# Kernel optimization log

Hardware: AMD Instinct MI355X
Metric: run time of the kernel (lower is better)

## Reference

```python
import jax, jax.numpy as jnp
import numpy as np

BN_EPS = 1e-5
EPS = 1e-6


def _conv(x, w, pad, dil):
    # NCHW dilated conv, stride 1, no bias (matches nn.Conv2d(bias=False))
    return jax.lax.conv_general_dilated(
        x, w, window_strides=(1, 1), padding=[(pad, pad), (pad, pad)],
        rhs_dilation=(dil, dil), dimension_numbers=('NCHW', 'OIHW', 'NCHW'))


def _bn_relu(x, s, b, m, v):
    # eval-mode batchnorm (running stats) + relu
    inv = (s / jnp.sqrt(v + BN_EPS))[None, :, None, None]
    return jax.nn.relu((x - m[None, :, None, None]) * inv + b[None, :, None, None])


def _l2n(x):
    # l2_norm over channel dim (dim=-2 of [B,C,N]); no eps, as in source
    return x / jnp.linalg.norm(x, axis=1, keepdims=True)


def _forward(x, w1, w2, w3, w4, bn_scale, bn_bias, bn_mean, bn_var,
             wq, bq, wk, bk, wv, bv, gamma):
    B, C, H, W = x.shape
    N = H * W
    # HASP: four dilated-conv branches (dilations 1,6,12,18), concat to 128 ch
    specs = [(w1, 0, 1), (w2, 6, 6), (w3, 12, 12), (w4, 18, 18)]
    branches = [_bn_relu(_conv(x, w, p, d), bn_scale[i], bn_bias[i],
                         bn_mean[i], bn_var[i])
                for i, (w, p, d) in enumerate(specs)]
    x_q = jnp.concatenate(branches, axis=1)  # [B,128,H,W]
    # 1x1 convs as channel GEMMs
    Q = (jnp.einsum('oi,bihw->bohw', wq[:, :, 0, 0], x_q)
         + bq[None, :, None, None]).reshape(B, -1, N)  # [B,16,N]
    K = (jnp.einsum('oi,bihw->bohw', wk[:, :, 0, 0], x)
         + bk[None, :, None, None]).reshape(B, -1, N)  # [B,16,N]
    V = (jnp.einsum('oi,bihw->bohw', wv[:, :, 0, 0], x)
         + bv[None, :, None, None]).reshape(B, -1, N)  # [B,128,N]
    Qn = _l2n(Q).transpose(0, 2, 1)  # [B,N,16]
    Kn = _l2n(K)                     # [B,16,N]
    tailor = 1.0 / (N + jnp.einsum('bnm,bm->bn', Qn, Kn.sum(-1) + EPS))  # [B,N]
    vsum = V.sum(-1)[:, :, None]                      # [B,128,1]
    mat = jnp.einsum('bmn,bcn->bmc', Kn, V)           # [B,16,128]
    msum = vsum + jnp.einsum('bnm,bmc->bcn', Qn, mat)  # [B,128,N]
    out = (msum * tailor[:, None, :]).reshape(B, C, H, W)
    return gamma * out


def setup_inputs() -> dict:
    key = jax.random.key(0)
    ks = jax.random.split(key, 12)
    B, C, H, W = 8, 128, 128, 128
    M = 16  # in_places // scale
    d = {
        'x': jax.random.normal(ks[0], (B, C, H, W), jnp.float32),
        'w1': jax.random.normal(ks[1], (32, 128, 1, 1), jnp.float32) * 0.05,
        'w2': jax.random.normal(ks[2], (32, 128, 3, 3), jnp.float32) * 0.05,
        'w3': jax.random.normal(ks[3], (32, 128, 3, 3), jnp.float32) * 0.05,
        'w4': jax.random.normal(ks[4], (32, 128, 3, 3), jnp.float32) * 0.05,
        'bn_scale': jnp.ones((4, 32), jnp.float32),
        'bn_bias': jnp.zeros((4, 32), jnp.float32),
        'bn_mean': jnp.zeros((4, 32), jnp.float32),
        'bn_var': jnp.ones((4, 32), jnp.float32),
        'wq': jax.random.normal(ks[5], (M, 128, 1, 1), jnp.float32) * 0.05,
        'bq': jax.random.normal(ks[6], (M,), jnp.float32) * 0.05,
        'wk': jax.random.normal(ks[7], (M, 128, 1, 1), jnp.float32) * 0.05,
        'bk': jax.random.normal(ks[8], (M,), jnp.float32) * 0.05,
        'wv': jax.random.normal(ks[9], (C, 128, 1, 1), jnp.float32) * 0.05,
        'bv': jax.random.normal(ks[10], (C,), jnp.float32) * 0.05,
        'gamma': jax.random.uniform(ks[11], (1,), jnp.float32),
    }
    return d


def reference(x, w1, w2, w3, w4, bn_scale, bn_bias, bn_mean, bn_var,
              wq, bq, wk, bk, wv, bv, gamma):
    return _forward(x, w1, w2, w3, w4, bn_scale, bn_bias, bn_mean, bn_var,
                    wq, bq, wk, bk, wv, bv, gamma)
```

## Files before the change

kernel.cpp:

```cpp
#include <hip/hip_runtime.h>
#include <hip/hip_bf16.h>
#include <math.h>

#define NPIX   16384
#define BATCH  8
#define BN_EPS 1e-5f
#define EPS_V  1e-6f

typedef __attribute__((ext_vector_type(8))) short bf16x8;
typedef __attribute__((ext_vector_type(4))) float f32x4;
typedef const __attribute__((address_space(1))) unsigned int* gas_ptr;
typedef __attribute__((address_space(3))) unsigned int* las_ptr;

#define OFF_K     ((size_t)0)
#define OFF_PART2 ((size_t)8192)
#define OFF_W1F   ((size_t)2097152)
#define OFF_WKT   ((size_t)2101248)
#define OFF_WVT   ((size_t)2103296)
#define OFF_BF    ((size_t)2119680)
#define OFF_PART  ((size_t)2119808)
#define OFF_STATS ((size_t)3242112)
#define BASE_END  ((size_t)3259648)
#define OFF_WBT   BASE_END
#define OFF_XT    ((size_t)3314976)
#define OFF_WVB   ((size_t)11703584)
#define OFF_ZROW  ((size_t)11711776)
#define NEW_END   ((size_t)11713824)
#define OFF_SQ    OFF_XT
#define OFF_TL    ((size_t)(OFF_XT + 2097152))
#define OFF_W24T  BASE_END

__device__ inline unsigned short f2bf(float f) {
  union { float f; unsigned int u; } v; v.f = f;
  unsigned int r = (v.u + 0x7FFFu + ((v.u >> 16) & 1u)) >> 16;
  return (unsigned short)r;
}

__global__ void prep_common_kernel(const float* __restrict__ w1,
                                   const float* __restrict__ bns, const float* __restrict__ bnb,
                                   const float* __restrict__ bnm, const float* __restrict__ bnv,
                                   const float* __restrict__ wk, const float* __restrict__ wv,
                                   float* __restrict__ w1f, float* __restrict__ wkt,
                                   float* __restrict__ wvt, float* __restrict__ bf) {
  int tid = blockIdx.x * blockDim.x + threadIdx.x;
  int nt  = gridDim.x * blockDim.x;
  for (int i = tid; i < 128; i += nt) {
    float inv = bns[i] * rsqrtf(bnv[i] + BN_EPS);
    bf[i] = bnb[i] - bnm[i] * inv;
  }
  for (int i = tid; i < 4096; i += nt) {
    int c = i >> 5, o = i & 31;
    float inv = bns[o] * rsqrtf(bnv[o] + BN_EPS);
    w1f[i] = w1[o * 128 + c] * inv;
  }
  for (int i = tid; i < 2048; i += nt) {
    int c = i >> 4, m = i & 15;
    wkt[i] = wk[m * 128 + c];
  }
  for (int i = tid; i < 16384; i += nt) {
    int c = i >> 7, o = i & 127;
    wvt[i] = wv[o * 128 + c];
  }
}

__global__ void prep_convb_kernel(const float* __restrict__ w1,
                                  const float* __restrict__ w2, const float* __restrict__ w3,
                                  const float* __restrict__ w4,
                                  const float* __restrict__ bns, const float* __restrict__ bnv,
                                  const float* __restrict__ wk, const float* __restrict__ wv,
                                  unsigned short* __restrict__ wbtr,
                                  unsigned short* __restrict__ wvbr,
                                  unsigned short* __restrict__ wxbr,
                                  unsigned short* __restrict__ zrow) {
  int tid = blockIdx.x * blockDim.x + threadIdx.x;
  int nt  = gridDim.x * blockDim.x;
  for (int i = tid; i < 4096; i += nt) zrow[i] = 0;
  for (int i = tid; i < 16384; i += nt) {
    int e = i & 7, lane = (i >> 3) & 63, f = (i >> 9) & 7, q = i >> 12;
    int oc = f * 16 + (lane & 15);
    int c  = q * 32 + (lane >> 4) * 8 + e;
    wvbr[i] = f2bf(wv[oc * 128 + c]);
  }
  for (int i = tid; i < 6144; i += nt) {
    int e = i & 7, lane = (i >> 3) & 63, ct = i >> 9;
    int tile = ct % 3, q = ct / 3;
    int c = q * 32 + (lane >> 4) * 8 + e;
    float val;
    if (tile < 2) {
      int oc = tile * 16 + (lane & 15);
      val = w1[oc * 128 + c] * (bns[oc] * rsqrtf(bnv[oc] + BN_EPS));
    } else {
      val = wk[(lane & 15) * 128 + c];
    }
    wxbr[i] = f2bf(val);
  }
  for (int i = tid; i < 110592; i += nt) {
    int br = i / 36864;
    int r  = i - br * 36864;
    int tap  = r >> 12;
    int r2   = r & 4095;
    int q    = r2 >> 10;
    int r3   = r2 & 1023;
    int pair = r3 >> 9;
    int r4   = r3 & 511;
    int lane = r4 >> 3, e = r4 & 7;
    int oc = pair * 16 + (lane & 15);
    int c  = q * 32 + (lane >> 4) * 8 + e;
    const float* w = (br == 0) ? w2 : ((br == 1) ? w3 : w4);
    int bo = (br + 1) * 32 + oc;
    float inv = bns[bo] * rsqrtf(bnv[bo] + BN_EPS);
    wbtr[i] = f2bf(w[(oc * 128 + c) * 9 + tap] * inv);
  }
}

__global__ void prep_convf_kernel(const float* __restrict__ w2, const float* __restrict__ w3,
                                  const float* __restrict__ w4,
                                  const float* __restrict__ bns, const float* __restrict__ bnv,
                                  float* __restrict__ w24t) {
  int tid = blockIdx.x * blockDim.x + threadIdx.x;
  int nt  = gridDim.x * blockDim.x;
  for (int i = tid; i < 110592; i += nt) {
    int br  = i / 36864;
    int rem = i - br * 36864;
    int c   = rem / 288;
    int k   = (rem % 288) >> 5;
    int o   = rem & 31;
    const float* w = (br == 0) ? w2 : ((br == 1) ? w3 : w4);
    int bo = (br + 1) * 32 + o;
    float inv = bns[bo] * rsqrtf(bnv[bo] + BN_EPS);
    w24t[i] = w[(o * 128 + c) * 9 + k] * inv;
  }
}

__global__ __launch_bounds__(256) void a0_kernel(const float* __restrict__ x,
                                                 unsigned short* __restrict__ xt) {
  __shared__ unsigned short Ts[64][132];
  int t   = threadIdx.x;
  int b   = blockIdx.y;
  int px0 = blockIdx.x * 64;
  const float* xb = x + (size_t)b * 128 * NPIX;
  int p = t & 63, cq = t >> 6;
#pragma unroll 8
  for (int i = 0; i < 32; ++i) {
    int c = cq * 32 + i;
    Ts[p][c] = f2bf(xb[(size_t)c * NPIX + px0 + p]);
  }
  __syncthreads();
  int pw = t >> 2, cg = t & 3;
  unsigned short* dst = xt + ((size_t)(b * 4 + cg) * 16384 + px0 + pw) * 32;
  int sw = (pw >> 1) & 3;
#pragma unroll
  for (int k = 0; k < 8; ++k) {
    uint2 v = *(const uint2*)(&Ts[pw][cg * 32 + k * 4]);
    int cgs = (k >> 1) ^ sw;
    *(uint2*)(dst + cgs * 8 + (k & 1) * 4) = v;
  }
}

__global__ __launch_bounds__(256) void a1_kernel(const float* __restrict__ x,
                                                 const float* __restrict__ w1f,
                                                 const float* __restrict__ wkt,
                                                 const float* __restrict__ bfp,
                                                 const float* __restrict__ bk,
                                                 float* __restrict__ out,
                                                 float* __restrict__ Kbuf) {
  __shared__ float lw1[128 * 32];
  __shared__ float lwk[128 * 16];
  __shared__ float lbf[32];
  int t = threadIdx.x;
  for (int i = t; i < 4096; i += 256) lw1[i] = w1f[i];
  for (int i = t; i < 2048; i += 256) lwk[i] = wkt[i];
  if (t < 32) lbf[t] = bfp[t];
  __syncthreads();

  int b  = blockIdx.y;
  int px = blockIdx.x * 256 + t;
  const float* xb = x + (size_t)b * 128 * NPIX;

  float acc[48];
#pragma unroll
  for (int i = 0; i < 48; ++i) acc[i] = 0.f;

  for (int c = 0; c < 128; ++c) {
    float xv = xb[(size_t)c * NPIX + px];
    const float4* w1p = (const float4*)(lw1 + c * 32);
#pragma unroll
    for (int j = 0; j < 8; ++j) {
      float4 w = w1p[j];
      acc[j*4+0] = fmaf(w.x, xv, acc[j*4+0]);
      acc[j*4+1] = fmaf(w.y, xv, acc[j*4+1]);
      acc[j*4+2] = fmaf(w.z, xv, acc[j*4+2]);
      acc[j*4+3] = fmaf(w.w, xv, acc[j*4+3]);
    }
    const float4* wkp = (const float4*)(lwk + c * 16);
#pragma unroll
    for (int j = 0; j < 4; ++j) {
      float4 w = wkp[j];
      acc[32+j*4+0] = fmaf(w.x, xv, acc[32+j*4+0]);
      acc[32+j*4+1] = fmaf(w.y, xv, acc[32+j*4+1]);
      acc[32+j*4+2] = fmaf(w.z, xv, acc[32+j*4+2]);
      acc[32+j*4+3] = fmaf(w.w, xv, acc[32+j*4+3]);
    }
  }
#pragma unroll
  for (int o = 0; o < 32; ++o)
    out[((size_t)(b * 128 + o)) * NPIX + px] = fmaxf(acc[o] + lbf[o], 0.f);
#pragma unroll
  for (int m = 0; m < 16; ++m)
    Kbuf[((size_t)(b * 16 + m)) * NPIX + px] = acc[32 + m] + bk[m];
}

__global__ __launch_bounds__(256) void a2m_kernel(const unsigned short* __restrict__ xt,
                                                  const unsigned short* __restrict__ zrow,
                                                  const unsigned short* __restrict__ wbtr,
                                                  const float* __restrict__ bfp,
                                                  float* __restrict__ out) {
  __shared__ unsigned short sx[3 * 8192 + 8];
  int t    = threadIdx.x;
  int wave = t >> 6, lane = t & 63;
  int l15  = lane & 15, cg = lane >> 4;
  int idx  = blockIdx.x;
  int b    = idx & 7;
  int rest = idx >> 3;
  int h2   = rest & 63;
  int br   = rest >> 6;
  int d    = 6 * (br + 1);
  int h0   = h2 * 2;
  int j    = wave >> 1;
  int whalf = wave & 1;
  int p0   = whalf * 64;

  if (t == 0) *(uint4*)(sx + 24576) = make_uint4(0u, 0u, 0u, 0u);

  const unsigned short* wb    = wbtr + (size_t)br * 36864;
  const unsigned short* slabs = xt + (size_t)b * 4 * 524288;

  f32x4 acc[2][4];
#pragma unroll
  for (int i = 0; i < 2; ++i)
#pragma unroll
    for (int n = 0; n < 4; ++n) acc[i][n] = (f32x4){0.f, 0.f, 0.f, 0.f};

  int pxb[3], xorv[3];
#pragma unroll
  for (int kw = 0; kw < 3; ++kw) {
    pxb[kw]  = p0 + l15 + (kw - 1) * d;
    xorv[kw] = (cg ^ ((pxb[kw] >> 1) & 3)) << 4;
  }

  auto STAGE = [&](int s) {
    int q = s / 3, kh = s % 3;
    int srow = h0 + j + (kh - 1) * d;
    const unsigned short* rowsrc =
        ((unsigned)srow < 128u) ? (slabs + (size_t)q * 524288 + (size_t)srow * 4096)
                                : zrow;
    const unsigned short* gsrc = rowsrc + whalf * 2048 + lane * 8;
    unsigned short* lbase = sx + (s % 3) * 8192 + j * 4096 + whalf * 2048;
#pragma unroll
    for (int k = 0; k < 4; ++k)
      __builtin_amdgcn_global_load_lds((gas_ptr)(const void*)(gsrc + k * 512),
                                       (las_ptr)(void*)(lbase + k * 512), 16, 0, 0);
  };

  auto COMPUTE = [&](int s) {
    int q = s / 3, kh = s % 3;
    int bb = (s % 3) * 16384 + j * 8192;
    bf16x8 a[3][2];
#pragma unroll
    for (int kw = 0; kw < 3; ++kw) {
      int tap = kh * 3 + kw;
      const unsigned short* wt = wb + ((((size_t)tap * 4 + q) * 2) << 9);
      a[kw][0] = *(const bf16x8*)(wt + lane * 8);
      a[kw][1] = *(const bf16x8*)(wt + 512 + lane * 8);
    }
#pragma unroll
    for (int kw = 0; kw < 3; ++kw) {
      int base = bb + pxb[kw] * 64 + xorv[kw];
#pragma unroll
      for (int nf = 0; nf < 4; ++nf) {
        int px   = pxb[kw] + nf * 16;
        int addr = ((unsigned)px < 128u) ? (base + nf * 1024) : 49152;
        bf16x8 bv = *(const bf16x8*)((const char*)sx + addr);
        acc[0][nf] = __builtin_amdgcn_mfma_f32_16x16x32_bf16(a[kw][0], bv, acc[0][nf], 0, 0, 0);
        acc[1][nf] = __builtin_amdgcn_mfma_f32_16x16x32_bf16(a[kw][1], bv, acc[1][nf], 0, 0, 0);
      }
    }
  };

  STAGE(0);
  __syncthreads();
  for (int s = 0; s < 12; ++s) {
    if (s < 11) STAGE(s + 1);
    COMPUTE(s);
    __syncthreads();
  }

  int ocb = (br + 1) * 32;
  int pxw = (h0 + j) * 128 + p0;
#pragma unroll
  for (int mf = 0; mf < 2; ++mf) {
#pragma unroll
    for (int r = 0; r < 4; ++r) {
      int oc = mf * 16 + cg * 4 + r;
      float bias = bfp[ocb + oc];
      float* op = out + ((size_t)(b * 128 + ocb + oc)) * NPIX + pxw + l15;
#pragma unroll
      for (int nf = 0; nf < 4; ++nf)
        op[nf * 16] = fmaxf(acc[mf][nf][r] + bias, 0.f);
    }
  }
}

__global__ __launch_bounds__(256) void a2f_kernel(const float* __restrict__ x,
                                                  const float* __restrict__ w24t,
                                                  const float* __restrict__ bfp,
                                                  float* __restrict__ out) {
  int t  = threadIdx.x;
  int og = t & 3;
  int pg = (t >> 2) & 15;
  int r  = t >> 6;
  int br = blockIdx.z;
  int b  = blockIdx.y;
  int h  = blockIdx.x * 4 + r;
  int d  = 6 * (br + 1);

  const float* wt = w24t + (size_t)br * 36864;
  const float* bf = bfp + (br + 1) * 32;
  const float* xb = x + (size_t)b * 128 * NPIX;
  int w0 = pg << 3;

  float acc[8][8];
#pragma unroll
  for (int p = 0; p < 8; ++p)
#pragma unroll
    for (int o = 0; o < 8; ++o) acc[p][o] = 0.f;

  for (int c = 0; c < 128; ++c) {
    const float* xc = xb + (size_t)c * NPIX;
    const float* wc = wt + c * 288;
#pragma unroll
    for (int kh = 0; kh < 3; ++kh) {
      int row = h + (kh - 1) * d;
      if ((unsigned)row >= 128u) continue;
      const float* xr = xc + row * 128;
#pragma unroll
      for (int kw = 0; kw < 3; ++kw) {
        int wb = w0 + (kw - 1) * d;
        float xv[8];
        if (wb >= 0 && wb <= 120) {
          const float2* p2 = (const float2*)(xr + wb);
#pragma unroll
          for (int jj = 0; jj < 4; ++jj) {
            float2 v = p2[jj];
            xv[2*jj] = v.x; xv[2*jj+1] = v.y;
          }
        } else {
#pragma unroll
          for (int jj = 0; jj < 8; ++jj) {
            int ww = wb + jj;
            xv[jj] = ((unsigned)ww < 128u) ? xr[ww] : 0.f;
          }
        }
        const float4* wp = (const float4*)(wc + (kh * 3 + kw) * 32 + og * 8);
        float4 wa = wp[0], wbv = wp[1];
        float wr[8] = {wa.x, wa.y, wa.z, wa.w, wbv.x, wbv.y, wbv.z, wbv.w};
#pragma unroll
        for (int p = 0; p < 8; ++p)
#pragma unroll
          for (int o = 0; o < 8; ++o)
            acc[p][o] = fmaf(xv[p], wr[o], acc[p][o]);
      }
    }
  }

  int chbase = (br + 1) * 32 + og * 8;
  int n = h * 128 + w0;
#pragma unroll
  for (int o = 0; o < 8; ++o) {
    float bias = bf[og * 8 + o];
    float* op = out + ((size_t)(b * 128 + chbase + o)) * NPIX + n;
    float4 v0 = make_float4(fmaxf(acc[0][o] + bias, 0.f), fmaxf(acc[1][o] + bias, 0.f),
                            fmaxf(acc[2][o] + bias, 0.f), fmaxf(acc[3][o] + bias, 0.f));
    float4 v1 = make_float4(fmaxf(acc[4][o] + bias, 0.f), fmaxf(acc[5][o] + bias, 0.f),
                            fmaxf(acc[6][o] + bias, 0.f), fmaxf(acc[7][o] + bias, 0.f));
    ((float4*)op)[0] = v0;
    ((float4*)op)[1] = v1;
  }
}

__global__ __launch_bounds__(256) void cm_kernel(const unsigned short* __restrict__ xt,
                                                 const unsigned short* __restrict__ wvbr,
                                                 const unsigned short* __restrict__ wxbr,
                                                 const float* __restrict__ bv,
                                                 const float* __restrict__ bfp,
                                                 const float* __restrict__ bk,
                                                 float* __restrict__ out,
                                                 float* __restrict__ part1,
                                                 float* __restrict__ part2) {
  __shared__ __align__(16) unsigned short Vl[128 * 136];
  __shared__ __align__(16) unsigned short knl[16 * 136];
  int t    = threadIdx.x;
  int idx  = blockIdx.x;
  int b    = idx & 7;
  int blk  = idx >> 3;
  int wave = t >> 6, lane = t & 63;
  int l15  = lane & 15, cg = lane >> 4;
  int ocb  = wave * 32;
  int pbase = blk << 7;
  int cgsw = (cg ^ ((l15 >> 1) & 3)) << 3;

  float bvr[2][4];
#pragma unroll
  for (int mf = 0; mf < 2; ++mf)
#pragma unroll
    for (int r = 0; r < 4; ++r) bvr[mf][r] = bv[ocb + mf * 16 + cg * 4 + r];

  float xb4[4];
#pragma unroll
  for (int r = 0; r < 4; ++r) xb4[r] = 0.f;
  if (wave == 0) {
#pragma unroll
    for (int r = 0; r < 4; ++r) xb4[r] = bfp[cg * 4 + r];
  } else if (wave == 1) {
#pragma unroll
    for (int r = 0; r < 4; ++r) xb4[r] = bfp[16 + cg * 4 + r];
  } else if (wave == 2) {
#pragma unroll
    for (int r = 0; r < 4; ++r) xb4[r] = bk[cg * 4 + r];
  }
  int xwave = (wave < 3) ? wave : 0;

  float kr[4] = {0.f, 0.f, 0.f, 0.f};
  float sv[2][4];
#pragma unroll
  for (int mf = 0; mf < 2; ++mf)
#pragma unroll
    for (int r = 0; r < 4; ++r) sv[mf][r] = 0.f;
  f32x4 am[2];
  am[0] = (f32x4){0.f,0.f,0.f,0.f};
  am[1] = (f32x4){0.f,0.f,0.f,0.f};

#pragma unroll
  for (int hf = 0; hf < 2; ++hf) {
    f32x4 vacc[2][4];
    f32x4 xacc[4];
#pragma unroll
    for (int i = 0; i < 2; ++i)
#pragma unroll
      for (int n = 0; n < 4; ++n) vacc[i][n] = (f32x4){0.f,0.f,0.f,0.f};
#pragma unroll
    for (int n = 0; n < 4; ++n) xacc[n] = (f32x4){0.f,0.f,0.f,0.f};

#pragma unroll
    for (int cc = 0; cc < 4; ++cc) {
      const unsigned short* xq = xt + ((size_t)(b * 4 + cc) * 16384 + pbase) * 32;
      bf16x8 a0 = *(const bf16x8*)(wvbr + ((cc * 8 + wave * 2 + 0) << 9) + lane * 8);
      bf16x8 a1 = *(const bf16x8*)(wvbr + ((cc * 8 + wave * 2 + 1) << 9) + lane * 8);
      bf16x8 ax = *(const bf16x8*)(wxbr + ((cc * 3 + xwave) << 9) + lane * 8);
#pragma unroll
      for (int nf = 0; nf < 4; ++nf) {
        int nfg = hf * 4 + nf;
        bf16x8 bx = *(const bf16x8*)(xq + (size_t)(nfg * 16 + l15) * 32 + cgsw);
        vacc[0][nf] = __builtin_amdgcn_mfma_f32_16x16x32_bf16(a0, bx, vacc[0][nf], 0, 0, 0);
        vacc[1][nf] = __builtin_amdgcn_mfma_f32_16x16x32_bf16(a1, bx, vacc[1][nf], 0, 0, 0);
        if (wave < 3)
          xacc[nf] = __builtin_amdgcn_mfma_f32_16x16x32_bf16(ax, bx, xacc[nf], 0, 0, 0);
      }
    }

#pragma unroll
    for (int mf = 0; mf < 2; ++mf) {
#pragma unroll
      for (int r = 0; r < 4; ++r) {
        float s = 0.f;
#pragma unroll
        for (int nf = 0; nf < 4; ++nf) s += vacc[mf][nf][r];
        sv[mf][r] += s;
        int c = ocb + mf * 16 + cg * 4 + r;
#pragma unroll
        for (int nf = 0; nf < 4; ++nf)
          Vl[c * 136 + (hf * 4 + nf) * 16 + l15] = f2bf(vacc[mf][nf][r] + bvr[mf][r]);
      }
    }

    if (wave < 2) {
#pragma unroll
      for (int r = 0; r < 4; ++r) {
        int oc = wave * 16 + cg * 4 + r;
        float* op = out + ((size_t)(b * 128 + oc)) * NPIX + pbase + l15;
#pragma unroll
        for (int nf = 0; nf < 4; ++nf)
          op[(hf * 4 + nf) * 16] = fmaxf(xacc[nf][r] + xb4[r], 0.f);
      }
    } else if (wave == 2) {
#pragma unroll
      for (int nf = 0; nf < 4; ++nf) {
        int nfg = hf * 4 + nf;
        float kq[4]; float s2 = 0.f;
#pragma unroll
        for (int r = 0; r < 4; ++r) {
          kq[r] = xacc[nf][r] + xb4[r];
          s2 = fmaf(kq[r], kq[r], s2);
        }
        s2 += __shfl_xor(s2, 16);
        s2 += __shfl_xor(s2, 32);
        float inv = rsqrtf(s2);
#pragma unroll
        for (int r = 0; r < 4; ++r) {
          float kn = kq[r] * inv;
          knl[(cg * 4 + r) * 136 + nfg * 16 + l15] = f2bf(kn);
          kr[r] += kn;
        }
      }
    }
  }
  __syncthreads();

#pragma unroll
  for (int ks = 0; ks < 4; ++ks) {
    bf16x8 af = *(const bf16x8*)(knl + l15 * 136 + ks * 32 + cg * 8);
    bf16x8 b0 = *(const bf16x8*)(Vl + (size_t)(ocb + l15) * 136 + ks * 32 + cg * 8);
    bf16x8 b1 = *(const bf16x8*)(Vl + (size_t)(ocb + 16 + l15) * 136 + ks * 32 + cg * 8);
    am[0] = __builtin_amdgcn_mfma_f32_16x16x32_bf16(af, b0, am[0], 0, 0, 0);
    am[1] = __builtin_amdgcn_mfma_f32_16x16x32_bf16(af, b1, am[1], 0, 0, 0);
  }

  float* pp = (blk < 64) ? (part1 + ((size_t)b * 64 + blk) * 2192)
                         : (part2 + ((size_t)b * 64 + (blk - 64)) * 2192);
#pragma unroll
  for (int nf2 = 0; nf2 < 2; ++nf2)
#pragma unroll
    for (int r = 0; r < 4; ++r)
      pp[(cg * 4 + r) * 128 + ocb + nf2 * 16 + l15] = am[nf2][r];
#pragma unroll
  for (int off = 1; off < 16; off <<= 1) {
#pragma unroll
    for (int mf = 0; mf < 2; ++mf)
#pragma unroll
      for (int r = 0; r < 4; ++r)
        sv[mf][r] += __shfl_xor(sv[mf][r], off);
  }
  if (l15 == 0) {
#pragma unroll
    for (int mf = 0; mf < 2; ++mf)
#pragma unroll
      for (int r = 0; r < 4; ++r) {
        int c = ocb + mf * 16 + cg * 4 + r;
        pp[2048 + c] = sv[mf][r] + 128.f * bv[c];
      }
  }
  if (wave == 2) {
#pragma unroll
    for (int off = 1; off < 16; off <<= 1) {
#pragma unroll
      for (int r = 0; r < 4; ++r)
        kr[r] += __shfl_xor(kr[r], off);
    }
    if (l15 == 0) {
#pragma unroll
      for (int r = 0; r < 4; ++r)
        pp[2048 + 128 + cg * 4 + r] = kr[r];
    }
  }
}

__global__ __launch_bounds__(256) void cf_kernel(const float* __restrict__ x,
                                                 const float* __restrict__ bv,
                                                 const float* __restrict__ Kbuf,
                                                 const float* __restrict__ wvt,
                                                 float* __restrict__ part) {
  __shared__ float Vl[128 * 129];
  __shared__ float knl[16 * 132];
  int t   = threadIdx.x;
  int b   = blockIdx.y;
  int blk = blockIdx.x;
  const float* Kb = Kbuf + (size_t)b * 16 * NPIX;
  const float* xb = x + (size_t)b * 128 * NPIX;

  int m_own = t & 15;
  int c0    = (t >> 4) << 3;
  int pxg   = t & 15;

  float bvr[8];
#pragma unroll
  for (int jj = 0; jj < 8; ++jj) bvr[jj] = bv[c0 + jj];

  float macc[8] = {0,0,0,0,0,0,0,0};
  float vs[8]   = {0,0,0,0,0,0,0,0};
  float ksum[16];
#pragma unroll
  for (int m = 0; m < 16; ++m) ksum[m] = 0.f;

  for (int tile = blk; tile < 128; tile += 64) {
    __syncthreads();
    int pbase = tile << 7;

    if (t < 128) {
      float kv[16]; float ss = 0.f;
#pragma unroll
      for (int m = 0; m < 16; ++m) {
        kv[m] = Kb[(size_t)m * NPIX + pbase + t];
        ss = fmaf(kv[m], kv[m], ss);
      }
      float inv = rsqrtf(ss);
#pragma unroll
      for (int m = 0; m < 16; ++m) {
        float kn = kv[m] * inv;
        knl[m * 132 + t] = kn;
        ksum[m] += kn;
      }
    }

    float v[8][8];
#pragma unroll
    for (int i = 0; i < 8; ++i)
#pragma unroll
      for (int jj = 0; jj < 8; ++jj) v[i][jj] = 0.f;
    int px0 = pbase + (pxg << 3);
    for (int k = 0; k < 128; ++k) {
      const float4* xp = (const float4*)(xb + (size_t)k * NPIX + px0);
      float4 xa = xp[0], xc4 = xp[1];
      const float4* wp = (const float4*)(wvt + k * 128 + c0);
      float4 wa = wp[0], wc4 = wp[1];
      float xv[8] = {xa.x, xa.y, xa.z, xa.w, xc4.x, xc4.y, xc4.z, xc4.w};
      float wr[8] = {wa.x, wa.y, wa.z, wa.w, wc4.x, wc4.y, wc4.z, wc4.w};
#pragma unroll
      for (int i = 0; i < 8; ++i)
#pragma unroll
        for (int jj = 0; jj < 8; ++jj)
          v[i][jj] = fmaf(wr[i], xv[jj], v[i][jj]);
    }
#pragma unroll
    for (int i = 0; i < 8; ++i)
#pragma unroll
      for (int jj = 0; jj < 8; ++jj)
        Vl[(c0 + i) * 129 + (pxg << 3) + jj] = v[i][jj] + bvr[i];
    __syncthreads();

    for (int px = 0; px < 128; ++px) {
      float knv = knl[m_own * 132 + px];
      float vv[8];
#pragma unroll
      for (int jj = 0; jj < 8; ++jj) vv[jj] = Vl[(c0 + jj) * 129 + px];
#pragma unroll
      for (int jj = 0; jj < 8; ++jj) macc[jj] = fmaf(knv, vv[jj], macc[jj]);
      if (m_own == 0) {
#pragma unroll
        for (int jj = 0; jj < 8; ++jj) vs[jj] += vv[jj];
      }
    }
  }

  int blkid = b * 64 + blk;
  float* pp = part + (size_t)blkid * 2192;
#pragma unroll
  for (int jj = 0; jj < 8; ++jj) pp[m_own * 128 + c0 + jj] = macc[jj];
  if (m_own == 0) {
#pragma unroll
    for (int jj = 0; jj < 8; ++jj) pp[2048 + c0 + jj] = vs[jj];
  }
  __syncthreads();
  if (t < 128) {
#pragma unroll
    for (int m = 0; m < 16; ++m) knl[m * 132 + t] = ksum[m];
  }
  __syncthreads();
  if (t < 16) {
    float s = 0.f;
    for (int i = 0; i < 128; ++i) s += knl[t * 132 + i];
    pp[2048 + 128 + t] = s;
  }
}

__global__ void reduce_kernel(const float* __restrict__ part, float* __restrict__ stats) {
  int b = blockIdx.y, t = threadIdx.x;
  int e = blockIdx.x * 256 + t;
  if (e >= 2192) return;
  const float* pp = part + (size_t)b * 64 * 2192;
  float s = 0.f;
  for (int g = 0; g < 64; ++g) s += pp[(size_t)g * 2192 + e];
  stats[(size_t)b * 2192 + e] = s;
}

__global__ void reduce2_kernel(const float* __restrict__ part1,
                               const float* __restrict__ part2,
                               float* __restrict__ stats) {
  int b = blockIdx.y, t = threadIdx.x;
  int e = blockIdx.x * 256 + t;
  if (e >= 2192) return;
  const float* p1 = part1 + (size_t)b * 64 * 2192;
  const float* p2 = part2 + (size_t)b * 64 * 2192;
  float s = 0.f;
  for (int g = 0; g < 64; ++g) s += p1[(size_t)g * 2192 + e];
  for (int g = 0; g < 64; ++g) s += p2[(size_t)g * 2192 + e];
  stats[(size_t)b * 2192 + e] = s;
}

__global__ __launch_bounds__(256) void d1_kernel(const float* __restrict__ stats,
                                                 const float* __restrict__ wq,
                                                 const float* __restrict__ bq,
                                                 const float* __restrict__ gamma,
                                                 const float* __restrict__ out,
                                                 float* __restrict__ sq,
                                                 float* __restrict__ tlb) {
  __shared__ float wql[128 * 16];
  __shared__ float ksl[16];
  int t = threadIdx.x;
  int b = blockIdx.y;
  const float* st = stats + (size_t)b * 2192;
  for (int i = t; i < 2048; i += 256) {
    int m = i >> 7, c = i & 127;
    wql[c * 16 + m] = wq[m * 128 + c];
  }
  if (t < 16) ksl[t] = st[2048 + 128 + t] + EPS_V;
  __syncthreads();

  int px = blockIdx.x * 256 + t;
  const float* ob = out + (size_t)b * 128 * NPIX;

  float q[16];
#pragma unroll
  for (int m = 0; m < 16; ++m) q[m] = bq[m];
  for (int c = 0; c < 128; ++c) {
    float xv = ob[(size_t)c * NPIX + px];
    const float4* wp = (const float4*)(wql + c * 16);
#pragma unroll
    for (int jj = 0; jj < 4; ++jj) {
      float4 w = wp[jj];
      q[jj*4+0] = fmaf(w.x, xv, q[jj*4+0]);
      q[jj*4+1] = fmaf(w.y, xv, q[jj*4+1]);
      q[jj*4+2] = fmaf(w.z, xv, q[jj*4+2]);
      q[jj*4+3] = fmaf(w.w, xv, q[jj*4+3]);
    }
  }
  float ss = 0.f;
#pragma unroll
  for (int m = 0; m < 16; ++m) ss = fmaf(q[m], q[m], ss);
  float inv = rsqrtf(ss);
#pragma unroll
  for (int m = 0; m < 16; ++m) q[m] *= inv;
  float den = (float)NPIX;
#pragma unroll
  for (int m = 0; m < 16; ++m) den = fmaf(q[m], ksl[m], den);
  float tl = gamma[0] / den;

  tlb[(size_t)b * NPIX + px] = tl;
#pragma unroll
  for (int m = 0; m < 16; ++m)
    sq[((size_t)(b * 16 + m)) * NPIX + px] = tl * q[m];
}

__global__ __launch_bounds__(256) void d2_kernel(const float* __restrict__ stats,
                                                 const float* __restrict__ sq,
                                                 const float* __restrict__ tlb,
                                                 float* __restrict__ out) {
  __shared__ float matl[128 * 16];
  __shared__ float vsl[128];
  int t = threadIdx.x;
  int b = blockIdx.y;
  const float* st = stats + (size_t)b * 2192;
  for (int i = t; i < 2048; i += 256) {
    int m = i >> 7, c = i & 127;
    matl[c * 16 + m] = st[i];
  }
  if (t < 128) vsl[t] = st[2048 + t];
  __syncthreads();

  int px = blockIdx.x * 256 + t;
  float* ob = out + (size_t)b * 128 * NPIX;

  float tlv = tlb[(size_t)b * NPIX + px];
  float sv[16];
#pragma unroll
  for (int m = 0; m < 16; ++m)
    sv[m] = sq[((size_t)(b * 16 + m)) * NPIX + px];

  for (int c = 0; c < 128; ++c) {
    float s = vsl[c] * tlv;
    const float4* mp = (const float4*)(matl + c * 16);
#pragma unroll
    for (int jj = 0; jj < 4; ++jj) {
      float4 w = mp[jj];
      s = fmaf(w.x, sv[jj*4+0], s);
      s = fmaf(w.y, sv[jj*4+1], s);
      s = fmaf(w.z, sv[jj*4+2], s);
      s = fmaf(w.w, sv[jj*4+3], s);
    }
    ob[(size_t)c * NPIX + px] = s;
  }
}

__global__ __launch_bounds__(256) void df_kernel(const float* __restrict__ stats,
                                                 const float* __restrict__ wq,
                                                 const float* __restrict__ bq,
                                                 const float* __restrict__ gamma,
                                                 float* __restrict__ out) {
  __shared__ float matl[128 * 16];
  __shared__ float wql[128 * 16];
  __shared__ float vsl[128];
  __shared__ float ksl[16];
  int t = threadIdx.x;
  int b = blockIdx.y;
  const float* st = stats + (size_t)b * 2192;
  for (int i = t; i < 2048; i += 256) {
    int m = i >> 7, c = i & 127;
    matl[c * 16 + m] = st[i];
    wql[c * 16 + m]  = wq[m * 128 + c];
  }
  if (t < 128) vsl[t] = st[2048 + t];
  if (t < 16)  ksl[t] = st[2048 + 128 + t] + EPS_V;
  __syncthreads();

  int px = blockIdx.x * 256 + t;
  float* ob = out + (size_t)b * 128 * NPIX;

  float q[16];
#pragma unroll
  for (int m = 0; m < 16; ++m) q[m] = bq[m];
  for (int c = 0; c < 128; ++c) {
    float xv = ob[(size_t)c * NPIX + px];
    const float4* wp = (const float4*)(wql + c * 16);
#pragma unroll
    for (int jj = 0; jj < 4; ++jj) {
      float4 w = wp[jj];
      q[jj*4+0] = fmaf(w.x, xv, q[jj*4+0]);
      q[jj*4+1] = fmaf(w.y, xv, q[jj*4+1]);
      q[jj*4+2] = fmaf(w.z, xv, q[jj*4+2]);
      q[jj*4+3] = fmaf(w.w, xv, q[jj*4+3]);
    }
  }
  float ss = 0.f;
#pragma unroll
  for (int m = 0; m < 16; ++m) ss = fmaf(q[m], q[m], ss);
  float inv = rsqrtf(ss);
#pragma unroll
  for (int m = 0; m < 16; ++m) q[m] *= inv;
  float den = (float)NPIX;
#pragma unroll
  for (int m = 0; m < 16; ++m) den = fmaf(q[m], ksl[m], den);
  float tl = gamma[0] / den;

  for (int c = 0; c < 128; ++c) {
    float s = vsl[c];
    const float4* mp = (const float4*)(matl + c * 16);
#pragma unroll
    for (int jj = 0; jj < 4; ++jj) {
      float4 w = mp[jj];
      s = fmaf(w.x, q[jj*4+0], s);
      s = fmaf(w.y, q[jj*4+1], s);
      s = fmaf(w.z, q[jj*4+2], s);
      s = fmaf(w.w, q[jj*4+3], s);
    }
    ob[(size_t)c * NPIX + px] = tl * s;
  }
}

extern "C" void kernel_launch(void* const* d_in, const int* in_sizes, int n_in,
                              void* d_out, int out_size, void* d_ws, size_t ws_size,
                              hipStream_t stream) {
  (void)in_sizes; (void)n_in; (void)out_size;
  const float* x   = (const float*)d_in[0];
  const float* w1  = (const float*)d_in[1];
  const float* w2  = (const float*)d_in[2];
  const float* w3  = (const float*)d_in[3];
  const float* w4  = (const float*)d_in[4];
  const float* bns = (const float*)d_in[5];
  const float* bnb = (const float*)d_in[6];
  const float* bnm = (const float*)d_in[7];
  const float* bnv = (const float*)d_in[8];
  const float* wq  = (const float*)d_in[9];
  const float* bq  = (const float*)d_in[10];
  const float* wk  = (const float*)d_in[11];
  const float* bk  = (const float*)d_in[12];
  const float* wv  = (const float*)d_in[13];
  const float* bv  = (const float*)d_in[14];
  const float* gm  = (const float*)d_in[15];
  float* ws  = (float*)d_ws;
  float* out = (float*)d_out;

  float* Kbuf = ws + OFF_K;
  float* w1f  = ws + OFF_W1F;
  float* wkt  = ws + OFF_WKT;
  float* wvt  = ws + OFF_WVT;
  float* bfp  = ws + OFF_BF;
  float* part = ws + OFF_PART;
  float* stat = ws + OFF_STATS;

  prep_common_kernel<<<64, 256, 0, stream>>>(w1, bns, bnb, bnm, bnv, wk, wv,
                                             w1f, wkt, wvt, bfp);

  bool use_mfma = ws_size >= NEW_END * sizeof(float);
  if (use_mfma) {
    unsigned short* wbtr = (unsigned short*)(ws + OFF_WBT);
    unsigned short* xt   = (unsigned short*)(ws + OFF_XT);
    unsigned short* wvbr = (unsigned short*)(ws + OFF_WVB);
    unsigned short* zrow = (unsigned short*)(ws + OFF_ZROW);
    unsigned short* wxbr = (unsigned short*)(ws + OFF_K);
    float* part2 = ws + OFF_PART2;
    float* sq  = ws + OFF_SQ;
    float* tlb = ws + OFF_TL;
    prep_convb_kernel<<<64, 256, 0, stream>>>(w1, w2, w3, w4, bns, bnv, wk, wv,
                                              wbtr, wvbr, wxbr, zrow);
    a0_kernel<<<dim3(256, 8), 256, 0, stream>>>(x, xt);
    a2m_kernel<<<dim3(1536), 256, 0, stream>>>(xt, zrow, wbtr, bfp, out);
    cm_kernel<<<dim3(1024), 256, 0, stream>>>(xt, wvbr, wxbr, bv, bfp, bk, out, part, part2);
    reduce2_kernel<<<dim3(9, 8), 256, 0, stream>>>(part, part2, stat);
    d1_kernel<<<dim3(64, 8), 256, 0, stream>>>(stat, wq, bq, gm, out, sq, tlb);
    d2_kernel<<<dim3(64, 8), 256, 0, stream>>>(stat, sq, tlb, out);
  } else {
    float* w24t = ws + OFF_W24T;
    prep_convf_kernel<<<64, 256, 0, stream>>>(w2, w3, w4, bns, bnv, w24t);
    a1_kernel<<<dim3(64, 8), 256, 0, stream>>>(x, w1f, wkt, bfp, bk, out, Kbuf);
    a2f_kernel<<<dim3(32, 8, 3), 256, 0, stream>>>(x, w24t, bfp, out);
    cf_kernel<<<dim3(64, 8), 256, 0, stream>>>(x, bv, Kbuf, wvt, part);
    reduce_kernel<<<dim3(9, 8), 256, 0, stream>>>(part, stat);
    df_kernel<<<dim3(64, 8), 256, 0, stream>>>(stat, wq, bq, gm, out);
  }
}
```

Before: 146.2 us.

## Prefetch conv stages two ahead and fuse final attention kernels into df_kernel

The dilated-conv MFMA kernel now stages two k-slices ahead instead of one. It swaps the full __syncthreads for a partial vmcnt wait plus a raw s_barrier, so global loads overlap more compute. Separately, the MFMA path drops the two-kernel d1/d2 epilogue, which wrote and reread scaled-Q and tailor buffers, and uses the single fused df_kernel from the fallback path. This removes one launch and the intermediate round trip through memory. The trade-off is more in-flight LDS staging, and a hand-tuned vmcnt count whose correctness depends on the exact number of loads STAGE issues.

```diff
diff --git a/kernel.cpp b/kernel.cpp
--- a/kernel.cpp
+++ b/kernel.cpp
@@ -26,8 +26,6 @@
 #define OFF_WVB   ((size_t)11703584)
 #define OFF_ZROW  ((size_t)11711776)
 #define NEW_END   ((size_t)11713824)
-#define OFF_SQ    OFF_XT
-#define OFF_TL    ((size_t)(OFF_XT + 2097152))
 #define OFF_W24T  BASE_END
 
 __device__ inline unsigned short f2bf(float f) {
@@ -288,11 +286,17 @@
   };
 
   STAGE(0);
+  STAGE(1);
   __syncthreads();
   for (int s = 0; s < 12; ++s) {
-    if (s < 11) STAGE(s + 1);
     COMPUTE(s);
-    __syncthreads();
+    if (s < 10) STAGE(s + 2);
+    if (s < 11) {
+      if (s < 10) asm volatile("s_waitcnt vmcnt(4)" ::: "memory");
+      else        asm volatile("s_waitcnt vmcnt(0)" ::: "memory");
+      __builtin_amdgcn_s_barrier();
+      __builtin_amdgcn_sched_barrier(0);
+    }
   }
 
   int ocb = (br + 1) * 32;
@@ -694,100 +698,6 @@
   for (int g = 0; g < 64; ++g) s += p1[(size_t)g * 2192 + e];
   for (int g = 0; g < 64; ++g) s += p2[(size_t)g * 2192 + e];
   stats[(size_t)b * 2192 + e] = s;
-}
-
-__global__ __launch_bounds__(256) void d1_kernel(const float* __restrict__ stats,
-                                                 const float* __restrict__ wq,
-                                                 const float* __restrict__ bq,
-                                                 const float* __restrict__ gamma,
-                                                 const float* __restrict__ out,
-                                                 float* __restrict__ sq,
-                                                 float* __restrict__ tlb) {
-  __shared__ float wql[128 * 16];
-  __shared__ float ksl[16];
-  int t = threadIdx.x;
-  int b = blockIdx.y;
-  const float* st = stats + (size_t)b * 2192;
-  for (int i = t; i < 2048; i += 256) {
-    int m = i >> 7, c = i & 127;
-    wql[c * 16 + m] = wq[m * 128 + c];
-  }
-  if (t < 16) ksl[t] = st[2048 + 128 + t] + EPS_V;
-  __syncthreads();
-
-  int px = blockIdx.x * 256 + t;
-  const float* ob = out + (size_t)b * 128 * NPIX;
-
-  float q[16];
-#pragma unroll
-  for (int m = 0; m < 16; ++m) q[m] = bq[m];
-  for (int c = 0; c < 128; ++c) {
-    float xv = ob[(size_t)c * NPIX + px];
-    const float4* wp = (const float4*)(wql + c * 16);
-#pragma unroll
-    for (int jj = 0; jj < 4; ++jj) {
-      float4 w = wp[jj];
-      q[jj*4+0] = fmaf(w.x, xv, q[jj*4+0]);
-      q[jj*4+1] = fmaf(w.y, xv, q[jj*4+1]);
-      q[jj*4+2] = fmaf(w.z, xv, q[jj*4+2]);
-      q[jj*4+3] = fmaf(w.w, xv, q[jj*4+3]);
-    }
-  }
-  float ss = 0.f;
-#pragma unroll
-  for (int m = 0; m < 16; ++m) ss = fmaf(q[m], q[m], ss);
-  float inv = rsqrtf(ss);
-#pragma unroll
-  for (int m = 0; m < 16; ++m) q[m] *= inv;
-  float den = (float)NPIX;
-#pragma unroll
-  for (int m = 0; m < 16; ++m) den = fmaf(q[m], ksl[m], den);
-  float tl = gamma[0] / den;
-
-  tlb[(size_t)b * NPIX + px] = tl;
-#pragma unroll
-  for (int m = 0; m < 16; ++m)
-    sq[((size_t)(b * 16 + m)) * NPIX + px] = tl * q[m];
-}
-
-__global__ __launch_bounds__(256) void d2_kernel(const float* __restrict__ stats,
-                                                 const float* __restrict__ sq,
-                                                 const float* __restrict__ tlb,
-                                                 float* __restrict__ out) {
-  __shared__ float matl[128 * 16];
-  __shared__ float vsl[128];
-  int t = threadIdx.x;
-  int b = blockIdx.y;
-  const float* st = stats + (size_t)b * 2192;
-  for (int i = t; i < 2048; i += 256) {
-    int m = i >> 7, c = i & 127;
-    matl[c * 16 + m] = st[i];
-  }
-  if (t < 128) vsl[t] = st[2048 + t];
-  __syncthreads();
-
-  int px = blockIdx.x * 256 + t;
-  float* ob = out + (size_t)b * 128 * NPIX;
-
-  float tlv = tlb[(size_t)b * NPIX + px];
-  float sv[16];
-#pragma unroll
-  for (int m = 0; m < 16; ++m)
-    sv[m] = sq[((size_t)(b * 16 + m)) * NPIX + px];
-
-  for (int c = 0; c < 128; ++c) {
-    float s = vsl[c] * tlv;
-    const float4* mp = (const float4*)(matl + c * 16);
-#pragma unroll
-    for (int jj = 0; jj < 4; ++jj) {
-      float4 w = mp[jj];
-      s = fmaf(w.x, sv[jj*4+0], s);
-      s = fmaf(w.y, sv[jj*4+1], s);
-      s = fmaf(w.z, sv[jj*4+2], s);
-      s = fmaf(w.w, sv[jj*4+3], s);
-    }
-    ob[(size_t)c * NPIX + px] = s;
-  }
 }
 
 __global__ __launch_bounds__(256) void df_kernel(const float* __restrict__ stats,
@@ -897,16 +807,13 @@
     unsigned short* zrow = (unsigned short*)(ws + OFF_ZROW);
     unsigned short* wxbr = (unsigned short*)(ws + OFF_K);
     float* part2 = ws + OFF_PART2;
-    float* sq  = ws + OFF_SQ;
-    float* tlb = ws + OFF_TL;
     prep_convb_kernel<<<64, 256, 0, stream>>>(w1, w2, w3, w4, bns, bnv, wk, wv,
                                               wbtr, wvbr, wxbr, zrow);
     a0_kernel<<<dim3(256, 8), 256, 0, stream>>>(x, xt);
     a2m_kernel<<<dim3(1536), 256, 0, stream>>>(xt, zrow, wbtr, bfp, out);
     cm_kernel<<<dim3(1024), 256, 0, stream>>>(xt, wvbr, wxbr, bv, bfp, bk, out, part, part2);
     reduce2_kernel<<<dim3(9, 8), 256, 0, stream>>>(part, part2, stat);
-    d1_kernel<<<dim3(64, 8), 256, 0, stream>>>(stat, wq, bq, gm, out, sq, tlb);
-    d2_kernel<<<dim3(64, 8), 256, 0, stream>>>(stat, sq, tlb, out);
+    df_kernel<<<dim3(64, 8), 256, 0, stream>>>(stat, wq, bq, gm, out);
   } else {
     float* w24t = ws + OFF_W24T;
     prep_convf_kernel<<<64, 256, 0, stream>>>(w2, w3, w4, bns, bnv, w24t);
```

Measured after the change: 138.5 us. -5.3%, faster.
